# Optimization experiments

Measured on AMD Instinct MI355X. Metric: run time of the kernel, lower is better.

Reference implementation:

```python
import jax, jax.numpy as jnp
import numpy as np

INPUT_SIZE = 1
HIDDEN = 64
B, T = 1024, 1024


def setup_inputs() -> dict:
    key = jax.random.key(0)
    ks = jax.random.split(key, 16)
    s = 1.0 / np.sqrt(HIDDEN)  # PyTorch LSTM init scale
    def u(k, shape):
        return jax.random.uniform(k, shape, jnp.float32, -s, s)
    x = jax.random.normal(ks[0], (B, T, INPUT_SIZE), jnp.float32)
    return {
        "x": x,
        # layer 0 (input_size -> hidden), gate order i,f,g,o stacked along 4H
        "W_ih0": u(ks[1], (4 * HIDDEN, INPUT_SIZE)),
        "W_hh0": u(ks[2], (4 * HIDDEN, HIDDEN)),
        "b_ih0": u(ks[3], (4 * HIDDEN,)),
        "b_hh0": u(ks[4], (4 * HIDDEN,)),
        # layer 1 (hidden -> hidden)
        "W_ih1": u(ks[5], (4 * HIDDEN, HIDDEN)),
        "W_hh1": u(ks[6], (4 * HIDDEN, HIDDEN)),
        "b_ih1": u(ks[7], (4 * HIDDEN,)),
        "b_hh1": u(ks[8], (4 * HIDDEN,)),
        # FC head: Linear(64,32) -> ReLU -> Linear(32,1)
        "fc1_w": u(ks[9], (HIDDEN // 2, HIDDEN)),
        "fc1_b": u(ks[10], (HIDDEN // 2,)),
        "fc2_w": u(ks[11], (1, HIDDEN // 2)),
        "fc2_b": u(ks[12], (1,)),
    }


def _lstm_layer(x_seq, W_ih, W_hh, b_ih, b_hh):
    """One LSTM layer over [B, T, D_in] -> hidden sequence [B, T, H]."""
    Bsz = x_seq.shape[0]
    H = W_hh.shape[1]
    # precompute input projection for all timesteps: [B, T, 4H]
    xW = jnp.einsum("btd,gd->btg", x_seq, W_ih) + b_ih + b_hh
    Whh_T = W_hh.T  # [H, 4H]

    def step(carry, xw_t):
        h, c = carry
        gates = xw_t + h @ Whh_T  # [B, 4H]
        i, f, g, o = jnp.split(gates, 4, axis=-1)
        i = jax.nn.sigmoid(i)
        f = jax.nn.sigmoid(f)
        g = jnp.tanh(g)
        o = jax.nn.sigmoid(o)
        c = f * c + i * g
        h = o * jnp.tanh(c)
        return (h, c), h

    h0 = jnp.zeros((Bsz, H), x_seq.dtype)
    (_, _), hs = jax.lax.scan(step, (h0, h0), jnp.swapaxes(xW, 0, 1))
    return jnp.swapaxes(hs, 0, 1)  # [B, T, H]


def reference(x, W_ih0, W_hh0, b_ih0, b_hh0, W_ih1, W_hh1, b_ih1, b_hh1,
              fc1_w, fc1_b, fc2_w, fc2_b):
    # 2-layer LSTM (inference: inter-layer dropout is identity)
    h1 = _lstm_layer(x, W_ih0, W_hh0, b_ih0, b_hh0)
    h2 = _lstm_layer(h1, W_ih1, W_hh1, b_ih1, b_hh1)
    last = h2[:, -1, :]  # [B, H]
    z = jax.nn.relu(last @ fc1_w.T + fc1_b)
    out = z @ fc2_w.T + fc2_b  # [B, 1]
    return out.squeeze(-1)  # [B]
```

## Files before the change

### kernel.cpp

```cpp
#include <hip/hip_runtime.h>

#define HID  64
#define SEQT 1024
#define NB   4

typedef _Float16 h8 __attribute__((ext_vector_type(8)));
typedef float    f4 __attribute__((ext_vector_type(4)));
typedef float    v2f __attribute__((ext_vector_type(2)));

__device__ __forceinline__ float rcpf(float x){ return __builtin_amdgcn_rcpf(x); }
__device__ __forceinline__ float sigm(float x){ return rcpf(1.0f + __expf(-x)); }
__device__ __forceinline__ float tanh_fast(float x){
    return 1.0f - 2.0f * rcpf(__expf(2.0f * x) + 1.0f);
}
__device__ __forceinline__ v2f pkfma(v2f a, v2f b, v2f c){
    return __builtin_elementwise_fma(a, b, c);
}

#define MFMA16(A,B,C) __builtin_amdgcn_mfma_f32_16x16x32_f16((A),(B),(C),0,0,0)

__device__ __forceinline__ h8 cvt8(const float* __restrict__ p) {
    float4 u = *(const float4*)p;
    float4 v = *(const float4*)(p + 4);
    h8 r;
    r[0] = (_Float16)u.x; r[1] = (_Float16)u.y;
    r[2] = (_Float16)u.z; r[3] = (_Float16)u.w;
    r[4] = (_Float16)v.x; r[5] = (_Float16)v.y;
    r[6] = (_Float16)v.z; r[7] = (_Float16)v.w;
    return r;
}

__global__ __launch_bounds__(512, 2)
void lstm2_v18(const float* __restrict__ x,
               const float* __restrict__ W_ih0, const float* __restrict__ W_hh0,
               const float* __restrict__ b_ih0, const float* __restrict__ b_hh0,
               const float* __restrict__ W_ih1, const float* __restrict__ W_hh1,
               const float* __restrict__ b_ih1, const float* __restrict__ b_hh1,
               const float* __restrict__ fc1_w, const float* __restrict__ fc1_b,
               const float* __restrict__ fc2_w, const float* __restrict__ fc2_b,
               float* __restrict__ out, int nblk)
{
    const int blk = blockIdx.x;
    if (blk >= nblk) return;
    const int tid = threadIdx.x;
    const int w   = tid >> 6;
    const int l   = tid & 63;
    const int r16 = l & 15;
    const int g4  = l >> 4;
    const int cc  = r16 & 3;
    const bool isCell = (w >= 4);
    const int cb  = w & 3;
    const int B0  = blk * NB;

    __shared__ __align__(16) _Float16 h1f[2][NB][80];
    __shared__ __align__(16) _Float16 h2f16[2][NB][80];
    __shared__ __align__(16) float G0[NB][260];
    __shared__ __align__(16) float G1[NB][260];
    __shared__ __align__(16) float h2fin[NB][64];

    h8 a0[4][2];
    h8 a1[4][4];
    if (!isCell) {
        #pragma unroll
        for (int tt = 0; tt < 4; ++tt) {
            const int row = 16 * (w + 4 * tt) + r16;
            #pragma unroll
            for (int ks = 0; ks < 2; ++ks) {
                a0[tt][ks]     = cvt8(W_hh0 + row * HID + ks * 32 + g4 * 8);
                a1[tt][ks]     = cvt8(W_ih1 + row * HID + ks * 32 + g4 * 8);
                a1[tt][2 + ks] = cvt8(W_hh1 + row * HID + ks * 32 + g4 * 8);
            }
        }
    }

    v2f bias0A, bias0B, bias1A, bias1B, wihA, wihB;
    if (isCell) {
        bias0A.x = b_ih0[l]       + b_hh0[l];
        bias0A.y = b_ih0[l + 64]  + b_hh0[l + 64];
        bias0B.x = b_ih0[l + 128] + b_hh0[l + 128];
        bias0B.y = b_ih0[l + 192] + b_hh0[l + 192];
        bias1A.x = b_ih1[l]       + b_hh1[l];
        bias1A.y = b_ih1[l + 64]  + b_hh1[l + 64];
        bias1B.x = b_ih1[l + 128] + b_hh1[l + 128];
        bias1B.y = b_ih1[l + 192] + b_hh1[l + 192];
        wihA.x = W_ih0[l];       wihA.y = W_ih0[l + 64];
        wihB.x = W_ih0[l + 128]; wihB.y = W_ih0[l + 192];
    }

    if (tid < 320) {
        ((int*)h1f)[tid] = 0; ((int*)h2f16)[tid] = 0;
    }
    const size_t xbase = (size_t)(B0 + cb) * SEQT;
    float xc = 0.0f, xcn = 0.0f;
    if (isCell) xc = x[xbase + l];
    float c1 = 0.0f, c2 = 0.0f;
    __syncthreads();

    const f4 z4 = {0.f, 0.f, 0.f, 0.f};

    auto step = [&](int t_, int P,
                    bool L0A, bool G1A, bool C0A, bool C1A, bool FIN) {
        const int RB1 = P ^ 1;
        f4 p0, p1, p2, p3;

        if (isCell) {
            if (((t_ & 63) == 0) && (t_ + 64 < SEQT))
                xcn = x[xbase + t_ + 64 + l];
            if (C1A) {
                v2f gA = {G1[cb][l],       G1[cb][l + 64]};
                v2f gB = {G1[cb][l + 128], G1[cb][l + 192]};
                v2f pA = gA + bias1A;
                v2f pB = gB + bias1B;
                float iv = sigm(pA.x), fv = sigm(pA.y);
                float gv = tanh_fast(pB.x), ov = sigm(pB.y);
                c2 = fmaf(fv, c2, iv * gv);
                float hv = ov * tanh_fast(c2);
                _Float16 hh = (_Float16)hv;
                h2f16[P][cb][l] = hh;
                if (FIN) h2fin[cb][l] = (float)hh;
            }
        } else {
            h8 b1h0, b1h1;
            if (L0A || G1A) {
                b1h0 = *(const h8*)&h1f[RB1][cc][g4 * 8];
                b1h1 = *(const h8*)&h1f[RB1][cc][32 + g4 * 8];
            }
            __builtin_amdgcn_s_setprio(1);
            if (L0A) {
                f4 e0 = MFMA16(a0[0][0], b1h0, z4);
                f4 e1 = MFMA16(a0[1][0], b1h0, z4);
                f4 e2 = MFMA16(a0[2][0], b1h0, z4);
                f4 e3 = MFMA16(a0[3][0], b1h0, z4);
                e0 = MFMA16(a0[0][1], b1h1, e0);
                e1 = MFMA16(a0[1][1], b1h1, e1);
                e2 = MFMA16(a0[2][1], b1h1, e2);
                e3 = MFMA16(a0[3][1], b1h1, e3);
                if (r16 < NB) {
                    *(f4*)&G0[r16][16 * w + 4 * g4]       = e0;
                    *(f4*)&G0[r16][16 * w + 64 + 4 * g4]  = e1;
                    *(f4*)&G0[r16][16 * w + 128 + 4 * g4] = e2;
                    *(f4*)&G0[r16][16 * w + 192 + 4 * g4] = e3;
                }
            }
            if (G1A) {
                p0 = MFMA16(a1[0][0], b1h0, z4);
                p1 = MFMA16(a1[1][0], b1h0, z4);
                p2 = MFMA16(a1[2][0], b1h0, z4);
                p3 = MFMA16(a1[3][0], b1h0, z4);
                p0 = MFMA16(a1[0][1], b1h1, p0);
                p1 = MFMA16(a1[1][1], b1h1, p1);
                p2 = MFMA16(a1[2][1], b1h1, p2);
                p3 = MFMA16(a1[3][1], b1h1, p3);
            }
            __builtin_amdgcn_s_setprio(0);
        }
        __syncthreads();

        if (isCell) {
            if (C0A) {
                v2f gA = {G0[cb][l],       G0[cb][l + 64]};
                v2f gB = {G0[cb][l + 128], G0[cb][l + 192]};
                const float xt = __shfl(xc, t_ & 63);
                v2f xt2 = {xt, xt};
                v2f pA = gA + pkfma(xt2, wihA, bias0A);
                v2f pB = gB + pkfma(xt2, wihB, bias0B);
                float iv = sigm(pA.x), fv = sigm(pA.y);
                float gv = tanh_fast(pB.x), ov = sigm(pB.y);
                c1 = fmaf(fv, c1, iv * gv);
                float hv = ov * tanh_fast(c1);
                h1f[P][cb][l] = (_Float16)hv;
            }
            if ((t_ & 63) == 63) xc = xcn;
        } else {
            if (G1A) {
                h8 b2h0 = *(const h8*)&h2f16[P][cc][g4 * 8];
                h8 b2h1 = *(const h8*)&h2f16[P][cc][32 + g4 * 8];
                __builtin_amdgcn_s_setprio(1);
                p0 = MFMA16(a1[0][2], b2h0, p0);
                p1 = MFMA16(a1[1][2], b2h0, p1);
                p2 = MFMA16(a1[2][2], b2h0, p2);
                p3 = MFMA16(a1[3][2], b2h0, p3);
                p0 = MFMA16(a1[0][3], b2h1, p0);
                p1 = MFMA16(a1[1][3], b2h1, p1);
                p2 = MFMA16(a1[2][3], b2h1, p2);
                p3 = MFMA16(a1[3][3], b2h1, p3);
                __builtin_amdgcn_s_setprio(0);
                if (r16 < NB) {
                    *(f4*)&G1[r16][16 * w + 4 * g4]       = p0;
                    *(f4*)&G1[r16][16 * w + 64 + 4 * g4]  = p1;
                    *(f4*)&G1[r16][16 * w + 128 + 4 * g4] = p2;
                    *(f4*)&G1[r16][16 * w + 192 + 4 * g4] = p3;
                }
            }
        }
        __syncthreads();
    };

    step(        0,    0, true,  false, true,  false, false);
    step(        1,    1, true,  true,  true,  false, false);
    #pragma unroll 1
    for (int t = 2; t < SEQT; t += 2) {
        step(t,      0, true,  true,  true,  true,  false);
        step(t + 1,  1, true,  true,  true,  true,  false);
    }
    step(     SEQT,    0, false, true,  false, true,  false);
    step( SEQT + 1,    1, false, false, false, true,  true );

    if (w < 4) {
        float z = 0.0f;
        if (l < 32) {
            float acc = fc1_b[l];
            const f4* hvp = (const f4*)h2fin[w];
            const f4* wvp = (const f4*)(fc1_w + l * HID);
            #pragma unroll
            for (int q = 0; q < 16; ++q) {
                f4 hq = hvp[q], wk = wvp[q];
                acc = fmaf(hq[0], wk[0], acc); acc = fmaf(hq[1], wk[1], acc);
                acc = fmaf(hq[2], wk[2], acc); acc = fmaf(hq[3], wk[3], acc);
            }
            z = fmaxf(acc, 0.0f) * fc2_w[l];
        }
        #pragma unroll
        for (int off = 32; off > 0; off >>= 1) z += __shfl_xor(z, off);
        if (l == 0) out[B0 + w] = z + fc2_b[0];
    }
}

extern "C" void kernel_launch(void* const* d_in, const int* in_sizes, int n_in,
                              void* d_out, int out_size, void* d_ws, size_t ws_size,
                              hipStream_t stream) {
    const float* x     = (const float*)d_in[0];
    const float* W_ih0 = (const float*)d_in[1];
    const float* W_hh0 = (const float*)d_in[2];
    const float* b_ih0 = (const float*)d_in[3];
    const float* b_hh0 = (const float*)d_in[4];
    const float* W_ih1 = (const float*)d_in[5];
    const float* W_hh1 = (const float*)d_in[6];
    const float* b_ih1 = (const float*)d_in[7];
    const float* b_hh1 = (const float*)d_in[8];
    const float* fc1_w = (const float*)d_in[9];
    const float* fc1_b = (const float*)d_in[10];
    const float* fc2_w = (const float*)d_in[11];
    const float* fc2_b = (const float*)d_in[12];
    float* out = (float*)d_out;

    const int batch = in_sizes[0] / SEQT;
    const int nblk  = batch / NB;
    dim3 grid(nblk), block(512);
    hipLaunchKernelGGL(lstm2_v18, grid, block, 0, stream,
                       x, W_ih0, W_hh0, b_ih0, b_hh0,
                       W_ih1, W_hh1, b_ih1, b_hh1,
                       fc1_w, fc1_b, fc2_w, fc2_b, out, nblk);
}
```

Measured before the change: 497.4 us.

## Interleave gate rows for vector gate reads and rebalance MFMA phases

Permutes the W_hh/W_ih weight rows so that the four gates of each hidden unit land next to each other in the G0/G1 shared buffers. Cell threads can then fetch all four gates with one float4 LDS read instead of four scalar reads. Half of the layer-1 input-projection MFMAs move from the first phase to the second phase to balance MFMA work across the two barriers, and cell waves now run at raised priority. Risks: re-reading the h1 operand in the second phase adds LDS traffic, and the reordering adds latency to the second phase.

```diff
diff --git a/kernel.cpp b/kernel.cpp
--- a/kernel.cpp
+++ b/kernel.cpp
@@ -12,9 +12,6 @@
 __device__ __forceinline__ float sigm(float x){ return rcpf(1.0f + __expf(-x)); }
 __device__ __forceinline__ float tanh_fast(float x){
     return 1.0f - 2.0f * rcpf(__expf(2.0f * x) + 1.0f);
-}
-__device__ __forceinline__ v2f pkfma(v2f a, v2f b, v2f c){
-    return __builtin_elementwise_fma(a, b, c);
 }
 
 #define MFMA16(A,B,C) __builtin_amdgcn_mfma_f32_16x16x32_f16((A),(B),(C),0,0,0)
@@ -31,7 +28,7 @@
 }
 
 __global__ __launch_bounds__(512, 2)
-void lstm2_v18(const float* __restrict__ x,
+void lstm2_v19(const float* __restrict__ x,
                const float* __restrict__ W_ih0, const float* __restrict__ W_hh0,
                const float* __restrict__ b_ih0, const float* __restrict__ b_hh0,
                const float* __restrict__ W_ih1, const float* __restrict__ W_hh1,
@@ -63,28 +60,25 @@
     if (!isCell) {
         #pragma unroll
         for (int tt = 0; tt < 4; ++tt) {
-            const int row = 16 * (w + 4 * tt) + r16;
+            const int rowP = 64 * (r16 & 3) + 16 * w + 4 * tt + (r16 >> 2);
             #pragma unroll
             for (int ks = 0; ks < 2; ++ks) {
-                a0[tt][ks]     = cvt8(W_hh0 + row * HID + ks * 32 + g4 * 8);
-                a1[tt][ks]     = cvt8(W_ih1 + row * HID + ks * 32 + g4 * 8);
-                a1[tt][2 + ks] = cvt8(W_hh1 + row * HID + ks * 32 + g4 * 8);
-            }
-        }
-    }
-
-    v2f bias0A, bias0B, bias1A, bias1B, wihA, wihB;
+                a0[tt][ks]     = cvt8(W_hh0 + rowP * HID + ks * 32 + g4 * 8);
+                a1[tt][ks]     = cvt8(W_ih1 + rowP * HID + ks * 32 + g4 * 8);
+                a1[tt][2 + ks] = cvt8(W_hh1 + rowP * HID + ks * 32 + g4 * 8);
+            }
+        }
+    }
+
+    float bias0v[4], bias1v[4], wih0v[4];
     if (isCell) {
-        bias0A.x = b_ih0[l]       + b_hh0[l];
-        bias0A.y = b_ih0[l + 64]  + b_hh0[l + 64];
-        bias0B.x = b_ih0[l + 128] + b_hh0[l + 128];
-        bias0B.y = b_ih0[l + 192] + b_hh0[l + 192];
-        bias1A.x = b_ih1[l]       + b_hh1[l];
-        bias1A.y = b_ih1[l + 64]  + b_hh1[l + 64];
-        bias1B.x = b_ih1[l + 128] + b_hh1[l + 128];
-        bias1B.y = b_ih1[l + 192] + b_hh1[l + 192];
-        wihA.x = W_ih0[l];       wihA.y = W_ih0[l + 64];
-        wihB.x = W_ih0[l + 128]; wihB.y = W_ih0[l + 192];
+        #pragma unroll
+        for (int r = 0; r < 4; ++r) {
+            const int grow = 64 * r + l;
+            bias0v[r] = b_ih0[grow] + b_hh0[grow];
+            bias1v[r] = b_ih1[grow] + b_hh1[grow];
+            wih0v[r]  = W_ih0[grow];
+        }
     }
 
     if (tid < 320) {
@@ -95,6 +89,7 @@
     if (isCell) xc = x[xbase + l];
     float c1 = 0.0f, c2 = 0.0f;
     __syncthreads();
+    if (isCell) __builtin_amdgcn_s_setprio(1);
 
     const f4 z4 = {0.f, 0.f, 0.f, 0.f};
 
@@ -107,12 +102,11 @@
             if (((t_ & 63) == 0) && (t_ + 64 < SEQT))
                 xcn = x[xbase + t_ + 64 + l];
             if (C1A) {
-                v2f gA = {G1[cb][l],       G1[cb][l + 64]};
-                v2f gB = {G1[cb][l + 128], G1[cb][l + 192]};
-                v2f pA = gA + bias1A;
-                v2f pB = gB + bias1B;
-                float iv = sigm(pA.x), fv = sigm(pA.y);
-                float gv = tanh_fast(pB.x), ov = sigm(pB.y);
+                f4 g = *(const f4*)&G1[cb][4 * l];
+                float iv = sigm(g[0] + bias1v[0]);
+                float fv = sigm(g[1] + bias1v[1]);
+                float gv = tanh_fast(g[2] + bias1v[2]);
+                float ov = sigm(g[3] + bias1v[3]);
                 c2 = fmaf(fv, c2, iv * gv);
                 float hv = ov * tanh_fast(c2);
                 _Float16 hh = (_Float16)hv;
@@ -136,21 +130,18 @@
                 e2 = MFMA16(a0[2][1], b1h1, e2);
                 e3 = MFMA16(a0[3][1], b1h1, e3);
                 if (r16 < NB) {
-                    *(f4*)&G0[r16][16 * w + 4 * g4]       = e0;
-                    *(f4*)&G0[r16][16 * w + 64 + 4 * g4]  = e1;
-                    *(f4*)&G0[r16][16 * w + 128 + 4 * g4] = e2;
-                    *(f4*)&G0[r16][16 * w + 192 + 4 * g4] = e3;
+                    const int u = 16 * w + g4;
+                    *(f4*)&G0[r16][4 * (u + 0)]  = e0;
+                    *(f4*)&G0[r16][4 * (u + 4)]  = e1;
+                    *(f4*)&G0[r16][4 * (u + 8)]  = e2;
+                    *(f4*)&G0[r16][4 * (u + 12)] = e3;
                 }
             }
             if (G1A) {
                 p0 = MFMA16(a1[0][0], b1h0, z4);
                 p1 = MFMA16(a1[1][0], b1h0, z4);
-                p2 = MFMA16(a1[2][0], b1h0, z4);
-                p3 = MFMA16(a1[3][0], b1h0, z4);
                 p0 = MFMA16(a1[0][1], b1h1, p0);
                 p1 = MFMA16(a1[1][1], b1h1, p1);
-                p2 = MFMA16(a1[2][1], b1h1, p2);
-                p3 = MFMA16(a1[3][1], b1h1, p3);
             }
             __builtin_amdgcn_s_setprio(0);
         }
@@ -158,14 +149,12 @@
 
         if (isCell) {
             if (C0A) {
-                v2f gA = {G0[cb][l],       G0[cb][l + 64]};
-                v2f gB = {G0[cb][l + 128], G0[cb][l + 192]};
+                f4 g = *(const f4*)&G0[cb][4 * l];
                 const float xt = __shfl(xc, t_ & 63);
-                v2f xt2 = {xt, xt};
-                v2f pA = gA + pkfma(xt2, wihA, bias0A);
-                v2f pB = gB + pkfma(xt2, wihB, bias0B);
-                float iv = sigm(pA.x), fv = sigm(pA.y);
-                float gv = tanh_fast(pB.x), ov = sigm(pB.y);
+                float iv = sigm(g[0] + fmaf(xt, wih0v[0], bias0v[0]));
+                float fv = sigm(g[1] + fmaf(xt, wih0v[1], bias0v[1]));
+                float gv = tanh_fast(g[2] + fmaf(xt, wih0v[2], bias0v[2]));
+                float ov = sigm(g[3] + fmaf(xt, wih0v[3], bias0v[3]));
                 c1 = fmaf(fv, c1, iv * gv);
                 float hv = ov * tanh_fast(c1);
                 h1f[P][cb][l] = (_Float16)hv;
@@ -173,9 +162,15 @@
             if ((t_ & 63) == 63) xc = xcn;
         } else {
             if (G1A) {
+                h8 b1h0 = *(const h8*)&h1f[RB1][cc][g4 * 8];
+                h8 b1h1 = *(const h8*)&h1f[RB1][cc][32 + g4 * 8];
                 h8 b2h0 = *(const h8*)&h2f16[P][cc][g4 * 8];
                 h8 b2h1 = *(const h8*)&h2f16[P][cc][32 + g4 * 8];
                 __builtin_amdgcn_s_setprio(1);
+                p2 = MFMA16(a1[2][0], b1h0, z4);
+                p3 = MFMA16(a1[3][0], b1h0, z4);
+                p2 = MFMA16(a1[2][1], b1h1, p2);
+                p3 = MFMA16(a1[3][1], b1h1, p3);
                 p0 = MFMA16(a1[0][2], b2h0, p0);
                 p1 = MFMA16(a1[1][2], b2h0, p1);
                 p2 = MFMA16(a1[2][2], b2h0, p2);
@@ -186,10 +181,11 @@
                 p3 = MFMA16(a1[3][3], b2h1, p3);
                 __builtin_amdgcn_s_setprio(0);
                 if (r16 < NB) {
-                    *(f4*)&G1[r16][16 * w + 4 * g4]       = p0;
-                    *(f4*)&G1[r16][16 * w + 64 + 4 * g4]  = p1;
-                    *(f4*)&G1[r16][16 * w + 128 + 4 * g4] = p2;
-                    *(f4*)&G1[r16][16 * w + 192 + 4 * g4] = p3;
+                    const int u = 16 * w + g4;
+                    *(f4*)&G1[r16][4 * (u + 0)]  = p0;
+                    *(f4*)&G1[r16][4 * (u + 4)]  = p1;
+                    *(f4*)&G1[r16][4 * (u + 8)]  = p2;
+                    *(f4*)&G1[r16][4 * (u + 12)] = p3;
                 }
             }
         }
@@ -247,7 +243,7 @@
     const int batch = in_sizes[0] / SEQT;
     const int nblk  = batch / NB;
     dim3 grid(nblk), block(512);
-    hipLaunchKernelGGL(lstm2_v18, grid, block, 0, stream,
+    hipLaunchKernelGGL(lstm2_v19, grid, block, 0, stream,
                        x, W_ih0, W_hh0, b_ih0, b_hh0,
                        W_ih1, W_hh1, b_ih1, b_hh1,
                        fc1_w, fc1_b, fc2_w, fc2_b, out, nblk);
```

New measurement: 529.1 us. 6.4% more time.
